# Optimization experiments

Measured on AMD Instinct MI355X. Metric: run time of the kernel, lower is better.

Reference implementation:

```python
import jax, jax.numpy as jnp
import numpy as np
from jax import lax

B, T, BYTE_LEN, EMB = 8, 4096, 8, 64
FILTERS = [(1, 4), (2, 8), (3, 12), (4, 16), (5, 20), (6, 24), (7, 28)]
LAST_DIM = sum(c for _, c in FILTERS)  # 112
OUT_DIM = 512


def setup_inputs() -> dict:
    key = jax.random.key(0)
    ks = jax.random.split(key, 32)
    inp = {"features": jax.random.normal(ks[0], (B, T, BYTE_LEN, EMB), dtype=jnp.float32)}
    for i, (w, c) in enumerate(FILTERS):
        inp[f"conv_w{i+1}"] = jax.random.normal(ks[1 + i], (c, EMB, w), dtype=jnp.float32) * 0.05
        inp[f"conv_b{i+1}"] = jax.random.normal(ks[8 + i], (c,), dtype=jnp.float32) * 0.05
    inp["hw_w1"] = jax.random.normal(ks[15], (2 * LAST_DIM, LAST_DIM), dtype=jnp.float32) * 0.05
    inp["hw_b1"] = jnp.concatenate([jnp.zeros(LAST_DIM), jnp.ones(LAST_DIM)]).astype(jnp.float32)
    inp["hw_w2"] = jax.random.normal(ks[16], (2 * LAST_DIM, LAST_DIM), dtype=jnp.float32) * 0.05
    inp["hw_b2"] = jnp.concatenate([jnp.zeros(LAST_DIM), jnp.ones(LAST_DIM)]).astype(jnp.float32)
    inp["proj_w"] = jax.random.normal(ks[17], (OUT_DIM, LAST_DIM), dtype=jnp.float32) * 0.05
    inp["proj_b"] = jax.random.normal(ks[18], (OUT_DIM,), dtype=jnp.float32) * 0.05
    return inp


def _conv_branch(x, w, b):
    # x: [N, EMB, BYTE_LEN], w: [out_c, EMB, width] -> max over time, relu -> [N, out_c]
    y = lax.conv_general_dilated(x, w, window_strides=(1,), padding='VALID',
                                 dimension_numbers=('NCH', 'OIH', 'NCH'))
    y = y + b[None, :, None]
    return jax.nn.relu(jnp.max(y, axis=-1))


def _highway_layer(x, w, b):
    p = x @ w.T + b
    proj_x, gate = jnp.split(p, 2, axis=-1)
    g = jax.nn.sigmoid(gate)
    return g * x + (1.0 - g) * jax.nn.relu(proj_x)


def reference(features, conv_w1, conv_w2, conv_w3, conv_w4, conv_w5, conv_w6, conv_w7,
              conv_b1, conv_b2, conv_b3, conv_b4, conv_b5, conv_b6, conv_b7,
              hw_w1, hw_b1, hw_w2, hw_b2, proj_w, proj_b):
    b, t, byte_len, emb = features.shape
    # transpose(2,3).view(-1, emb, byte_len)
    x = features.transpose(0, 1, 3, 2).reshape(-1, emb, byte_len)  # [B*T, EMB, BYTE_LEN]
    ws = [conv_w1, conv_w2, conv_w3, conv_w4, conv_w5, conv_w6, conv_w7]
    bs = [conv_b1, conv_b2, conv_b3, conv_b4, conv_b5, conv_b6, conv_b7]
    branches = [_conv_branch(x, w, bb) for w, bb in zip(ws, bs)]
    h = jnp.concatenate(branches, axis=-1)  # [B*T, LAST_DIM]
    h = _highway_layer(h, hw_w1, hw_b1)
    h = _highway_layer(h, hw_w2, hw_b2)
    out = h @ proj_w.T + proj_b  # [B*T, OUT_DIM]
    return out.reshape(b, t, -1)
```

## Files before the change

kernel.cpp:

```cpp
#include <hip/hip_runtime.h>

typedef __attribute__((ext_vector_type(8))) short short8;
typedef __attribute__((ext_vector_type(4))) float f32x4;

#define KDIM 512
#define NCT  30
#define CB_STRIDE 97
#define HT_OFF    28672
#define HT_STRIDE 132
#define RING_CH   8192

__device__ __forceinline__ unsigned short f2bf(float x) {
    unsigned u = __float_as_uint(x);
    return (unsigned short)((u + 0x7FFFu + ((u >> 16) & 1u)) >> 16);
}
__device__ __forceinline__ float bf2f(unsigned short h) {
    return __uint_as_float(((unsigned)h) << 16);
}

__device__ __forceinline__ void stage16(const void* g, void* l, int lane) {
    __builtin_amdgcn_global_load_lds(
        (const __attribute__((address_space(1))) unsigned int*)g,
        (__attribute__((address_space(3))) unsigned int*)l, 16, 0, 0);
}

__global__ void prep_kernel(const float* __restrict__ w1, const float* __restrict__ w2,
                            const float* __restrict__ w3, const float* __restrict__ w4,
                            const float* __restrict__ w5, const float* __restrict__ w6,
                            const float* __restrict__ w7, const float* __restrict__ hw1,
                            const float* __restrict__ hw2, const float* __restrict__ pw,
                            unsigned short* __restrict__ WC, unsigned short* __restrict__ W1s,
                            unsigned short* __restrict__ W2s, unsigned short* __restrict__ Ps) {
    int gid = blockIdx.x * 256 + threadIdx.x;
    if (gid < 245760) {
        int k = gid / 480, col = gid % 480;
        const float* wp; int cbnd, NP, C, W;
        if (col < 32)       { wp = w1; cbnd = 0;   NP = 8; C = 4;  W = 1; }
        else if (col < 96)  { wp = w2; cbnd = 32;  NP = 7; C = 8;  W = 2; }
        else if (col < 176) { wp = w3; cbnd = 96;  NP = 6; C = 12; W = 3; }
        else if (col < 256) { wp = w4; cbnd = 176; NP = 5; C = 16; W = 4; }
        else if (col < 336) { wp = w5; cbnd = 256; NP = 4; C = 20; W = 5; }
        else if (col < 416) { wp = w6; cbnd = 336; NP = 3; C = 24; W = 6; }
        else                { wp = w7; cbnd = 416; NP = 2; C = 28; W = 7; }
        int c2 = col - cbnd, oc = c2 / NP, p = c2 - oc * NP;
        int j = k >> 6, e = k & 63, dk = j - p;
        float v = 0.f;
        if (oc < C && dk >= 0 && dk < W) v = wp[(oc * 64 + e) * W + dk];
        int q = k >> 5, kr = k & 31;
        WC[q * 16384 + ((col >> 4) * 64 + ((kr >> 3) * 16 + (col & 15))) * 8 + (kr & 7)] = f2bf(v);
    } else if (gid < 245760 + 57344) {
        int x = gid - 245760;
        const float* src = (x < 28672) ? hw1 : hw2;
        unsigned short* dst = (x < 28672) ? W1s : W2s;
        if (x >= 28672) x -= 28672;
        int k = x / 224, n = x % 224;
        float v = (k < 112) ? src[n * 112 + k] : 0.f;
        int q = k >> 5, kr = k & 31;
        int h = (n >= 112) ? 1 : 0;
        int tt = (n >> 4) - h * 7;
        dst[(q * 2 + h) * 4096 + (tt * 64 + ((kr >> 3) * 16 + (n & 15))) * 8 + (kr & 7)] = f2bf(v);
    } else if (gid < 245760 + 57344 + 65536) {
        int x = gid - 303104;
        int k = x / 512, n = x % 512;
        float v = (k < 112) ? pw[n * 112 + k] : 0.f;
        int q = k >> 5, kr = k & 31;
        int c = q * 4 + (n >> 7);
        int tt = (n >> 4) & 7;
        Ps[c * 4096 + (tt * 64 + ((kr >> 3) * 16 + (n & 15))) * 8 + (kr & 7)] = f2bf(v);
    }
}

template <int T0, int NT>
__device__ __forceinline__ void dump_phase(float* Cb, const f32x4* acc, int w4, int lane) {
    int r0 = w4 * 16 + ((lane >> 4) * 4);
    int c0 = lane & 15;
#pragma unroll
    for (int tt = 0; tt < NT; ++tt)
#pragma unroll
        for (int r = 0; r < 4; ++r)
            Cb[(r0 + r) * CB_STRIDE + tt * 16 + c0] = acc[T0 + tt][r];
}

__device__ void reduce_phase(const float* Cb, unsigned short* ht, int tid,
                             int cA, int NPA, int choffA, int colbA, const float* cbA,
                             int cB, int NPB, int choffB, int colbB, const float* cbB) {
    int noc = cA + cB;
    for (int idx = tid; idx < 64 * noc; idx += 512) {
        int row = idx & 63, ocp = idx >> 6;
        bool isB = ocp >= cA;
        int oc = isB ? ocp - cA : ocp;
        int NP = isB ? NPB : NPA;
        int colb = isB ? colbB : colbA;
        int choff = isB ? choffB : choffA;
        const float* cb = isB ? cbB : cbA;
        const float* src = Cb + row * CB_STRIDE + colb + oc * NP;
        float m = src[0];
        for (int k = 1; k < NP; ++k) m = fmaxf(m, src[k]);
        float v = fmaxf(m + cb[oc], 0.f);
        ht[row * HT_STRIDE + choff + oc] = f2bf(v);
    }
}

template <int T0, int NT>
__device__ __forceinline__ void epi_phase(float* Cb, unsigned short* ht, const f32x4* acc,
                                          int tid, int wave, int lane,
                                          int cA, int NPA, int choffA, int colbA, const float* cbA,
                                          int cB, int NPB, int choffB, int colbB, const float* cbB) {
    for (int g = 0; g < 2; ++g) {
        if ((wave >> 2) == g) dump_phase<T0, NT>(Cb, acc, wave & 3, lane);
        __syncthreads();
        reduce_phase(Cb, ht + g * 64 * HT_STRIDE, tid,
                     cA, NPA, choffA, colbA, cbA, cB, NPB, choffB, colbB, cbB);
        __syncthreads();
    }
}

__global__ __launch_bounds__(512, 2) void fused_kernel(
        const float* __restrict__ feat, const unsigned short* __restrict__ WC,
        const float* cb0, const float* cb1, const float* cb2, const float* cb3,
        const float* cb4, const float* cb5, const float* cb6,
        const unsigned short* __restrict__ W1, const unsigned short* __restrict__ W2,
        const unsigned short* __restrict__ PW,
        const float* __restrict__ hb1, const float* __restrict__ hb2,
        const float* __restrict__ pb, float* __restrict__ out) {
    __shared__ __align__(16) char sm[65536];
    const int tid = threadIdx.x, lane = tid & 63, wave = tid >> 6;
    const int c0 = lane & 15, kq = lane >> 4;
    const int m0 = blockIdx.x * 128;
    f32x4 zero = {0.f, 0.f, 0.f, 0.f};

    const float* arow = feat + (size_t)(m0 + wave * 16 + c0) * KDIM + kq * 8;
    short8 af[16];
#pragma unroll
    for (int q = 0; q < 16; ++q) {
        float t[8];
        *(float4*)(t)     = *(const float4*)(arow + q * 32);
        *(float4*)(t + 4) = *(const float4*)(arow + q * 32 + 4);
        short8 v;
#pragma unroll
        for (int i = 0; i < 8; ++i) v[i] = (short)f2bf(t[i]);
        af[q] = v;
    }

    f32x4 acc[NCT];
#pragma unroll
    for (int t = 0; t < NCT; ++t) acc[t] = zero;

    for (int i = tid; i < 2048; i += 512)
        stage16(WC + i * 8, sm + (i - lane) * 16, lane);

#pragma unroll
    for (int q = 0; q < 16; ++q) {
        if (q < 15) {
            const unsigned short* src = WC + (q + 1) * 16384;
            char* dst = sm + ((q + 1) & 1) * 32768;
            for (int i = tid; i < 2048; i += 512)
                stage16(src + i * 8, dst + (i - lane) * 16, lane);
            asm volatile("s_waitcnt vmcnt(4)" ::: "memory");
        } else {
            asm volatile("s_waitcnt vmcnt(0)" ::: "memory");
        }
        __builtin_amdgcn_s_barrier();
        const char* bb = sm + (q & 1) * 32768;
#pragma unroll
        for (int t = 0; t < NCT; ++t) {
            short8 b = *(const short8*)(bb + (t * 64 + lane) * 16);
            acc[t] = __builtin_amdgcn_mfma_f32_16x16x32_bf16(af[q], b, acc[t], 0, 0, 0);
        }
        asm volatile("s_waitcnt lgkmcnt(0)" ::: "memory");
        __builtin_amdgcn_s_barrier();
    }

    float* Cb = (float*)sm;
    unsigned short* ht = (unsigned short*)(sm + HT_OFF);
    for (int i = tid; i < 2048; i += 512)
        ht[(i >> 4) * HT_STRIDE + 112 + (i & 15)] = 0;
    __syncthreads();
    epi_phase<0, 6>(Cb, ht, acc, tid, wave, lane, 4, 8, 0, 0, cb0, 8, 7, 4, 32, cb1);
    epi_phase<6, 5>(Cb, ht, acc, tid, wave, lane, 12, 6, 12, 0, cb2, 0, 1, 0, 0, cb2);
    epi_phase<11, 5>(Cb, ht, acc, tid, wave, lane, 16, 5, 24, 0, cb3, 0, 1, 0, 0, cb3);
    epi_phase<16, 5>(Cb, ht, acc, tid, wave, lane, 20, 4, 40, 0, cb4, 0, 1, 0, 0, cb4);
    epi_phase<21, 5>(Cb, ht, acc, tid, wave, lane, 24, 3, 60, 0, cb5, 0, 1, 0, 0, cb5);
    epi_phase<26, 4>(Cb, ht, acc, tid, wave, lane, 28, 2, 84, 0, cb6, 0, 1, 0, 0, cb6);

    char* ring = sm;
    short8 a2[4];
#pragma unroll
    for (int q = 0; q < 4; ++q)
        a2[q] = *(const short8*)((const char*)ht + (wave * 16 + c0) * 264 + q * 64 + kq * 16);

    stage16(W1 + tid * 8, ring + (tid - lane) * 16, lane);
    stage16(W1 + 4096 + tid * 8, ring + RING_CH + (tid - lane) * 16, lane);

    f32x4 acc2[14];
#pragma unroll
    for (int t = 0; t < 14; ++t) acc2[t] = zero;
#pragma unroll
    for (int i = 0; i < 8; ++i) {
        {
            const unsigned short* src = (i < 6) ? (W1 + (i + 2) * 4096) : (W2 + (i - 6) * 4096);
            char* dst = ring + ((i + 2) % 3) * RING_CH;
            stage16(src + tid * 8, dst + (tid - lane) * 16, lane);
        }
        asm volatile("s_waitcnt vmcnt(2)" ::: "memory");
        __builtin_amdgcn_s_barrier();
        const char* bb = ring + (i % 3) * RING_CH;
        const int q = i >> 1, h = i & 1;
#pragma unroll
        for (int tt = 0; tt < 7; ++tt) {
            short8 b = *(const short8*)(bb + (tt * 64 + lane) * 16);
            acc2[h * 7 + tt] = __builtin_amdgcn_mfma_f32_16x16x32_bf16(a2[q], b, acc2[h * 7 + tt], 0, 0, 0);
        }
        asm volatile("s_waitcnt lgkmcnt(0)" ::: "memory");
        __builtin_amdgcn_s_barrier();
    }

#pragma unroll
    for (int t = 0; t < 14; ++t) {
        float bp = hb1[t * 16 + c0], bg = hb1[112 + t * 16 + c0];
        (void)bg;
#pragma unroll
        for (int r = 0; r < 4; ++r) {
            int row = wave * 16 + kq * 4 + r;
            int col = t * 16 + c0;
            if (t < 7) {
                float px = acc2[t][r] + bp;
                float gt = acc2[t + 7][r] + hb1[112 + t * 16 + c0];
                float g = 1.f / (1.f + __expf(-gt));
                float hres = bf2f(ht[row * HT_STRIDE + col]);
                ht[row * HT_STRIDE + col] = f2bf(g * hres + (1.f - g) * fmaxf(px, 0.f));
            }
        }
    }
    asm volatile("s_waitcnt lgkmcnt(0)" ::: "memory");
    __builtin_amdgcn_s_barrier();

    short8 a3[4];
#pragma unroll
    for (int q = 0; q < 4; ++q)
        a3[q] = *(const short8*)((const char*)ht + (wave * 16 + c0) * 264 + q * 64 + kq * 16);

    f32x4 acc3[14];
#pragma unroll
    for (int t = 0; t < 14; ++t) acc3[t] = zero;
#pragma unroll
    for (int j = 0; j < 8; ++j) {
        {
            const unsigned short* src = (j < 6) ? (W2 + (j + 2) * 4096) : (PW + (j - 6) * 4096);
            char* dst = ring + ((j + 10) % 3) * RING_CH;
            stage16(src + tid * 8, dst + (tid - lane) * 16, lane);
        }
        asm volatile("s_waitcnt vmcnt(2)" ::: "memory");
        __builtin_amdgcn_s_barrier();
        const char* bb = ring + ((j + 8) % 3) * RING_CH;
        const int q = j >> 1, h = j & 1;
#pragma unroll
        for (int tt = 0; tt < 7; ++tt) {
            short8 b = *(const short8*)(bb + (tt * 64 + lane) * 16);
            acc3[h * 7 + tt] = __builtin_amdgcn_mfma_f32_16x16x32_bf16(a3[q], b, acc3[h * 7 + tt], 0, 0, 0);
        }
        asm volatile("s_waitcnt lgkmcnt(0)" ::: "memory");
        __builtin_amdgcn_s_barrier();
    }

#pragma unroll
    for (int t = 0; t < 7; ++t) {
        float bp = hb2[t * 16 + c0], bg = hb2[112 + t * 16 + c0];
#pragma unroll
        for (int r = 0; r < 4; ++r) {
            int row = wave * 16 + kq * 4 + r;
            int col = t * 16 + c0;
            float px = acc3[t][r] + bp;
            float gt = acc3[t + 7][r] + bg;
            float g = 1.f / (1.f + __expf(-gt));
            float hres = bf2f(ht[row * HT_STRIDE + col]);
            ht[row * HT_STRIDE + col] = f2bf(g * hres + (1.f - g) * fmaxf(px, 0.f));
        }
    }
    asm volatile("s_waitcnt lgkmcnt(0)" ::: "memory");
    __builtin_amdgcn_s_barrier();

    short8 a4[4];
#pragma unroll
    for (int q = 0; q < 4; ++q)
        a4[q] = *(const short8*)((const char*)ht + (wave * 16 + c0) * 264 + q * 64 + kq * 16);

    f32x4 acc4[32];
#pragma unroll
    for (int t = 0; t < 32; ++t) acc4[t] = zero;
#pragma unroll
    for (int k = 0; k < 16; ++k) {
        if (k < 14) {
            const unsigned short* src = PW + (k + 2) * 4096;
            char* dst = ring + ((k + 18) % 3) * RING_CH;
            stage16(src + tid * 8, dst + (tid - lane) * 16, lane);
            asm volatile("s_waitcnt vmcnt(2)" ::: "memory");
        } else if (k == 14) {
            asm volatile("s_waitcnt vmcnt(1)" ::: "memory");
        } else {
            asm volatile("s_waitcnt vmcnt(0)" ::: "memory");
        }
        __builtin_amdgcn_s_barrier();
        const char* bb = ring + ((k + 16) % 3) * RING_CH;
        const int q = k >> 2, e = k & 3;
#pragma unroll
        for (int tt = 0; tt < 8; ++tt) {
            short8 b = *(const short8*)(bb + (tt * 64 + lane) * 16);
            acc4[e * 8 + tt] = __builtin_amdgcn_mfma_f32_16x16x32_bf16(a4[q], b, acc4[e * 8 + tt], 0, 0, 0);
        }
        asm volatile("s_waitcnt lgkmcnt(0)" ::: "memory");
        __builtin_amdgcn_s_barrier();
    }

    float* ot = (float*)sm;
#pragma unroll
    for (int e = 0; e < 4; ++e) {
        __syncthreads();
#pragma unroll
        for (int tt = 0; tt < 8; ++tt) {
            int col = e * 128 + tt * 16 + c0;
            float b = pb[col];
#pragma unroll
            for (int r = 0; r < 4; ++r)
                ot[(wave * 16 + kq * 4 + r) * 128 + tt * 16 + c0] = acc4[e * 8 + tt][r] + b;
        }
        __syncthreads();
        for (int i = tid; i < 4096; i += 512) {
            int row = i >> 5, c = i & 31;
            *(float4*)(out + (size_t)(m0 + row) * 512 + e * 128 + c * 4) = ((const float4*)ot)[i];
        }
    }
}

extern "C" void kernel_launch(void* const* d_in, const int* in_sizes, int n_in,
                              void* d_out, int out_size, void* d_ws, size_t ws_size,
                              hipStream_t stream) {
    const float* feat = (const float*)d_in[0];
    const float* cw[7];
    const float* cb[7];
    for (int f = 0; f < 7; ++f) {
        cw[f] = (const float*)d_in[1 + 2 * f];
        cb[f] = (const float*)d_in[2 + 2 * f];
    }
    const float* hw_w1 = (const float*)d_in[15];
    const float* hw_b1 = (const float*)d_in[16];
    const float* hw_w2 = (const float*)d_in[17];
    const float* hw_b2 = (const float*)d_in[18];
    const float* pw    = (const float*)d_in[19];
    const float* pb    = (const float*)d_in[20];
    float* out = (float*)d_out;

    char* ws = (char*)d_ws;
    unsigned short* WC  = (unsigned short*)ws;
    unsigned short* W1s = (unsigned short*)(ws + 524288);
    unsigned short* W2s = (unsigned short*)(ws + 589824);
    unsigned short* Ps  = (unsigned short*)(ws + 655360);

    prep_kernel<<<1440, 256, 0, stream>>>(cw[0], cw[1], cw[2], cw[3], cw[4], cw[5], cw[6],
                                          hw_w1, hw_w2, pw, WC, W1s, W2s, Ps);
    fused_kernel<<<256, 512, 0, stream>>>(feat, WC, cb[0], cb[1], cb[2], cb[3], cb[4], cb[5], cb[6],
                                          W1s, W2s, Ps, hw_b1, hw_b2, pb, out);
}
```

Baseline: 191.7 us.

## Deepen conv weight pipeline, stage whole highway/proj weights in large LDS

The conv GEMM now keeps a 4-slot LDS ring with two chunks in flight instead of double-buffering, which drops the trailing barrier each iteration. The highway and projection weights are repacked into contiguous tiles and loaded whole into a 145KB dynamic LDS allocation, overlapping their loads with the conv epilogue and earlier layers. The aim is to remove most per-chunk barriers and load stalls. The output is now written straight from registers instead of being restaged through LDS. The large LDS footprint limits each CU to one block, down from two, and the direct output stores are less coalesced.

After: 198.7 us. 3.7% more time.

```diff
diff --git a/kernel.cpp b/kernel.cpp
--- a/kernel.cpp
+++ b/kernel.cpp
@@ -5,10 +5,14 @@
 
 #define KDIM 512
 #define NCT  30
-#define CB_STRIDE 97
-#define HT_OFF    28672
+#define SLOT      32768
+#define W1_OFF    0
+#define W2_OFF    57344
+#define CB_OFF    93952
+#define HT_OFF    114688
+#define LDS_TOTAL 148480
 #define HT_STRIDE 132
-#define RING_CH   8192
+#define CBS 81
 
 __device__ __forceinline__ unsigned short f2bf(float x) {
     unsigned u = __float_as_uint(x);
@@ -56,17 +60,13 @@
         int k = x / 224, n = x % 224;
         float v = (k < 112) ? src[n * 112 + k] : 0.f;
         int q = k >> 5, kr = k & 31;
-        int h = (n >= 112) ? 1 : 0;
-        int tt = (n >> 4) - h * 7;
-        dst[(q * 2 + h) * 4096 + (tt * 64 + ((kr >> 3) * 16 + (n & 15))) * 8 + (kr & 7)] = f2bf(v);
+        dst[(q * 14 + (n >> 4)) * 512 + ((kr >> 3) * 16 + (n & 15)) * 8 + (kr & 7)] = f2bf(v);
     } else if (gid < 245760 + 57344 + 65536) {
         int x = gid - 303104;
         int k = x / 512, n = x % 512;
         float v = (k < 112) ? pw[n * 112 + k] : 0.f;
         int q = k >> 5, kr = k & 31;
-        int c = q * 4 + (n >> 7);
-        int tt = (n >> 4) & 7;
-        Ps[c * 4096 + (tt * 64 + ((kr >> 3) * 16 + (n & 15))) * 8 + (kr & 7)] = f2bf(v);
+        Ps[(q * 32 + (n >> 4)) * 512 + ((kr >> 3) * 16 + (n & 15)) * 8 + (kr & 7)] = f2bf(v);
     }
 }
 
@@ -78,40 +78,33 @@
     for (int tt = 0; tt < NT; ++tt)
 #pragma unroll
         for (int r = 0; r < 4; ++r)
-            Cb[(r0 + r) * CB_STRIDE + tt * 16 + c0] = acc[T0 + tt][r];
-}
-
-__device__ void reduce_phase(const float* Cb, unsigned short* ht, int tid,
-                             int cA, int NPA, int choffA, int colbA, const float* cbA,
-                             int cB, int NPB, int choffB, int colbB, const float* cbB) {
-    int noc = cA + cB;
-    for (int idx = tid; idx < 64 * noc; idx += 512) {
-        int row = idx & 63, ocp = idx >> 6;
-        bool isB = ocp >= cA;
-        int oc = isB ? ocp - cA : ocp;
-        int NP = isB ? NPB : NPA;
-        int colb = isB ? colbB : colbA;
-        int choff = isB ? choffB : choffA;
-        const float* cb = isB ? cbB : cbA;
-        const float* src = Cb + row * CB_STRIDE + colb + oc * NP;
+            Cb[(r0 + r) * CBS + tt * 16 + c0] = acc[T0 + tt][r];
+}
+
+__device__ __forceinline__ void reduce_rows(const float* Cb, unsigned short* ht, int tid,
+                                            int c, int NP, int choff, const float* cb) {
+    for (int idx = tid; idx < 64 * c; idx += 512) {
+        int row = idx & 63, oc = idx >> 6;
+        const float* src = Cb + row * CBS + oc * NP;
         float m = src[0];
         for (int k = 1; k < NP; ++k) m = fmaxf(m, src[k]);
-        float v = fmaxf(m + cb[oc], 0.f);
-        ht[row * HT_STRIDE + choff + oc] = f2bf(v);
+        ht[row * HT_STRIDE + choff + oc] = f2bf(fmaxf(m + cb[oc], 0.f));
     }
 }
 
 template <int T0, int NT>
-__device__ __forceinline__ void epi_phase(float* Cb, unsigned short* ht, const f32x4* acc,
-                                          int tid, int wave, int lane,
-                                          int cA, int NPA, int choffA, int colbA, const float* cbA,
-                                          int cB, int NPB, int choffB, int colbB, const float* cbB) {
+__device__ __forceinline__ void epi_phase(char* smb, const f32x4* acc, int tid, int wave, int lane,
+                                          int c, int NP, int choff, const float* cb) {
+    float* Cb = (float*)(smb + CB_OFF);
+    unsigned short* ht = (unsigned short*)(smb + HT_OFF);
+#pragma unroll
     for (int g = 0; g < 2; ++g) {
         if ((wave >> 2) == g) dump_phase<T0, NT>(Cb, acc, wave & 3, lane);
-        __syncthreads();
-        reduce_phase(Cb, ht + g * 64 * HT_STRIDE, tid,
-                     cA, NPA, choffA, colbA, cbA, cB, NPB, choffB, colbB, cbB);
-        __syncthreads();
+        asm volatile("s_waitcnt lgkmcnt(0)" ::: "memory");
+        __builtin_amdgcn_s_barrier();
+        reduce_rows(Cb, ht + g * 64 * HT_STRIDE, tid, c, NP, choff, cb);
+        asm volatile("s_waitcnt lgkmcnt(0)" ::: "memory");
+        __builtin_amdgcn_s_barrier();
     }
 }
 
@@ -123,11 +116,12 @@
         const unsigned short* __restrict__ PW,
         const float* __restrict__ hb1, const float* __restrict__ hb2,
         const float* __restrict__ pb, float* __restrict__ out) {
-    __shared__ __align__(16) char sm[65536];
+    extern __shared__ __align__(16) char sm[];
     const int tid = threadIdx.x, lane = tid & 63, wave = tid >> 6;
     const int c0 = lane & 15, kq = lane >> 4;
     const int m0 = blockIdx.x * 128;
     f32x4 zero = {0.f, 0.f, 0.f, 0.f};
+    unsigned short* ht = (unsigned short*)(sm + HT_OFF);
 
     const float* arow = feat + (size_t)(m0 + wave * 16 + c0) * KDIM + kq * 8;
     short8 af[16];
@@ -148,120 +142,104 @@
 
     for (int i = tid; i < 2048; i += 512)
         stage16(WC + i * 8, sm + (i - lane) * 16, lane);
+    for (int i = tid; i < 2048; i += 512)
+        stage16(WC + 16384 + i * 8, sm + SLOT + (i - lane) * 16, lane);
 
 #pragma unroll
     for (int q = 0; q < 16; ++q) {
-        if (q < 15) {
-            const unsigned short* src = WC + (q + 1) * 16384;
-            char* dst = sm + ((q + 1) & 1) * 32768;
+        if (q < 14) {
+            const unsigned short* src = WC + (q + 2) * 16384;
+            char* dst = sm + ((q + 2) & 3) * SLOT;
             for (int i = tid; i < 2048; i += 512)
                 stage16(src + i * 8, dst + (i - lane) * 16, lane);
+            asm volatile("s_waitcnt vmcnt(8)" ::: "memory");
+        } else if (q == 14) {
             asm volatile("s_waitcnt vmcnt(4)" ::: "memory");
         } else {
             asm volatile("s_waitcnt vmcnt(0)" ::: "memory");
         }
         __builtin_amdgcn_s_barrier();
-        const char* bb = sm + (q & 1) * 32768;
+        const char* bb = sm + (q & 3) * SLOT;
 #pragma unroll
         for (int t = 0; t < NCT; ++t) {
             short8 b = *(const short8*)(bb + (t * 64 + lane) * 16);
             acc[t] = __builtin_amdgcn_mfma_f32_16x16x32_bf16(af[q], b, acc[t], 0, 0, 0);
         }
-        asm volatile("s_waitcnt lgkmcnt(0)" ::: "memory");
-        __builtin_amdgcn_s_barrier();
-    }
-
-    float* Cb = (float*)sm;
-    unsigned short* ht = (unsigned short*)(sm + HT_OFF);
+    }
+    asm volatile("s_waitcnt lgkmcnt(0)" ::: "memory");
+    __builtin_amdgcn_s_barrier();
+
+    for (int i = tid; i < 3584; i += 512)
+        stage16(W1 + i * 8, sm + W1_OFF + (i - lane) * 16, lane);
+
     for (int i = tid; i < 2048; i += 512)
         ht[(i >> 4) * HT_STRIDE + 112 + (i & 15)] = 0;
-    __syncthreads();
-    epi_phase<0, 6>(Cb, ht, acc, tid, wave, lane, 4, 8, 0, 0, cb0, 8, 7, 4, 32, cb1);
-    epi_phase<6, 5>(Cb, ht, acc, tid, wave, lane, 12, 6, 12, 0, cb2, 0, 1, 0, 0, cb2);
-    epi_phase<11, 5>(Cb, ht, acc, tid, wave, lane, 16, 5, 24, 0, cb3, 0, 1, 0, 0, cb3);
-    epi_phase<16, 5>(Cb, ht, acc, tid, wave, lane, 20, 4, 40, 0, cb4, 0, 1, 0, 0, cb4);
-    epi_phase<21, 5>(Cb, ht, acc, tid, wave, lane, 24, 3, 60, 0, cb5, 0, 1, 0, 0, cb5);
-    epi_phase<26, 4>(Cb, ht, acc, tid, wave, lane, 28, 2, 84, 0, cb6, 0, 1, 0, 0, cb6);
-
-    char* ring = sm;
+
+    epi_phase<0, 2>(sm, acc, tid, wave, lane, 4, 8, 0, cb0);
+    epi_phase<2, 4>(sm, acc, tid, wave, lane, 8, 7, 4, cb1);
+    epi_phase<6, 5>(sm, acc, tid, wave, lane, 12, 6, 12, cb2);
+    epi_phase<11, 5>(sm, acc, tid, wave, lane, 16, 5, 24, cb3);
+    epi_phase<16, 5>(sm, acc, tid, wave, lane, 20, 4, 40, cb4);
+    epi_phase<21, 5>(sm, acc, tid, wave, lane, 24, 3, 60, cb5);
+    epi_phase<26, 4>(sm, acc, tid, wave, lane, 28, 2, 84, cb6);
+
     short8 a2[4];
 #pragma unroll
     for (int q = 0; q < 4; ++q)
-        a2[q] = *(const short8*)((const char*)ht + (wave * 16 + c0) * 264 + q * 64 + kq * 16);
-
-    stage16(W1 + tid * 8, ring + (tid - lane) * 16, lane);
-    stage16(W1 + 4096 + tid * 8, ring + RING_CH + (tid - lane) * 16, lane);
+        a2[q] = *(const short8*)((const char*)ht + (wave * 16 + c0) * (HT_STRIDE * 2) + q * 64 + kq * 16);
+
+    for (int i = tid; i < 3584; i += 512)
+        stage16(W2 + i * 8, sm + W2_OFF + (i - lane) * 16, lane);
+    asm volatile("s_waitcnt vmcnt(7)" ::: "memory");
+    __builtin_amdgcn_s_barrier();
 
     f32x4 acc2[14];
 #pragma unroll
     for (int t = 0; t < 14; ++t) acc2[t] = zero;
 #pragma unroll
-    for (int i = 0; i < 8; ++i) {
-        {
-            const unsigned short* src = (i < 6) ? (W1 + (i + 2) * 4096) : (W2 + (i - 6) * 4096);
-            char* dst = ring + ((i + 2) % 3) * RING_CH;
-            stage16(src + tid * 8, dst + (tid - lane) * 16, lane);
-        }
-        asm volatile("s_waitcnt vmcnt(2)" ::: "memory");
-        __builtin_amdgcn_s_barrier();
-        const char* bb = ring + (i % 3) * RING_CH;
-        const int q = i >> 1, h = i & 1;
-#pragma unroll
-        for (int tt = 0; tt < 7; ++tt) {
-            short8 b = *(const short8*)(bb + (tt * 64 + lane) * 16);
-            acc2[h * 7 + tt] = __builtin_amdgcn_mfma_f32_16x16x32_bf16(a2[q], b, acc2[h * 7 + tt], 0, 0, 0);
-        }
-        asm volatile("s_waitcnt lgkmcnt(0)" ::: "memory");
-        __builtin_amdgcn_s_barrier();
-    }
-
-#pragma unroll
-    for (int t = 0; t < 14; ++t) {
+    for (int q = 0; q < 4; ++q)
+#pragma unroll
+        for (int t = 0; t < 14; ++t) {
+            short8 b = *(const short8*)(sm + W1_OFF + (q * 14 + t) * 1024 + lane * 16);
+            acc2[t] = __builtin_amdgcn_mfma_f32_16x16x32_bf16(a2[q], b, acc2[t], 0, 0, 0);
+        }
+
+#pragma unroll
+    for (int t = 0; t < 7; ++t) {
         float bp = hb1[t * 16 + c0], bg = hb1[112 + t * 16 + c0];
-        (void)bg;
 #pragma unroll
         for (int r = 0; r < 4; ++r) {
             int row = wave * 16 + kq * 4 + r;
             int col = t * 16 + c0;
-            if (t < 7) {
-                float px = acc2[t][r] + bp;
-                float gt = acc2[t + 7][r] + hb1[112 + t * 16 + c0];
-                float g = 1.f / (1.f + __expf(-gt));
-                float hres = bf2f(ht[row * HT_STRIDE + col]);
-                ht[row * HT_STRIDE + col] = f2bf(g * hres + (1.f - g) * fmaxf(px, 0.f));
-            }
-        }
-    }
-    asm volatile("s_waitcnt lgkmcnt(0)" ::: "memory");
+            float px = acc2[t][r] + bp;
+            float gt = acc2[t + 7][r] + bg;
+            float g = 1.f / (1.f + __expf(-gt));
+            float hres = bf2f(ht[row * HT_STRIDE + col]);
+            ht[row * HT_STRIDE + col] = f2bf(g * hres + (1.f - g) * fmaxf(px, 0.f));
+        }
+    }
+
+    short8 a3[4];
+#pragma unroll
+    for (int q = 0; q < 4; ++q)
+        a3[q] = *(const short8*)((const char*)ht + (wave * 16 + c0) * (HT_STRIDE * 2) + q * 64 + kq * 16);
+
+    asm volatile("s_waitcnt vmcnt(0)" ::: "memory");
     __builtin_amdgcn_s_barrier();
 
-    short8 a3[4];
-#pragma unroll
-    for (int q = 0; q < 4; ++q)
-        a3[q] = *(const short8*)((const char*)ht + (wave * 16 + c0) * 264 + q * 64 + kq * 16);
+    for (int i = tid; i < 2048; i += 512)
+        stage16(PW + i * 8, sm + (i - lane) * 16, lane);
 
     f32x4 acc3[14];
 #pragma unroll
     for (int t = 0; t < 14; ++t) acc3[t] = zero;
 #pragma unroll
-    for (int j = 0; j < 8; ++j) {
-        {
-            const unsigned short* src = (j < 6) ? (W2 + (j + 2) * 4096) : (PW + (j - 6) * 4096);
-            char* dst = ring + ((j + 10) % 3) * RING_CH;
-            stage16(src + tid * 8, dst + (tid - lane) * 16, lane);
-        }
-        asm volatile("s_waitcnt vmcnt(2)" ::: "memory");
-        __builtin_amdgcn_s_barrier();
-        const char* bb = ring + ((j + 8) % 3) * RING_CH;
-        const int q = j >> 1, h = j & 1;
-#pragma unroll
-        for (int tt = 0; tt < 7; ++tt) {
-            short8 b = *(const short8*)(bb + (tt * 64 + lane) * 16);
-            acc3[h * 7 + tt] = __builtin_amdgcn_mfma_f32_16x16x32_bf16(a3[q], b, acc3[h * 7 + tt], 0, 0, 0);
-        }
-        asm volatile("s_waitcnt lgkmcnt(0)" ::: "memory");
-        __builtin_amdgcn_s_barrier();
-    }
+    for (int q = 0; q < 4; ++q)
+#pragma unroll
+        for (int t = 0; t < 14; ++t) {
+            short8 b = *(const short8*)(sm + W2_OFF + (q * 14 + t) * 1024 + lane * 16);
+            acc3[t] = __builtin_amdgcn_mfma_f32_16x16x32_bf16(a3[q], b, acc3[t], 0, 0, 0);
+        }
 
 #pragma unroll
     for (int t = 0; t < 7; ++t) {
@@ -277,58 +255,45 @@
             ht[row * HT_STRIDE + col] = f2bf(g * hres + (1.f - g) * fmaxf(px, 0.f));
         }
     }
+
+    short8 a4[4];
+#pragma unroll
+    for (int q = 0; q < 4; ++q)
+        a4[q] = *(const short8*)((const char*)ht + (wave * 16 + c0) * (HT_STRIDE * 2) + q * 64 + kq * 16);
+
     asm volatile("s_waitcnt lgkmcnt(0)" ::: "memory");
     __builtin_amdgcn_s_barrier();
 
-    short8 a4[4];
-#pragma unroll
-    for (int q = 0; q < 4; ++q)
-        a4[q] = *(const short8*)((const char*)ht + (wave * 16 + c0) * 264 + q * 64 + kq * 16);
+#pragma unroll
+    for (int c = 1; c < 4; ++c)
+        for (int i = tid; i < 2048; i += 512)
+            stage16(PW + c * 16384 + i * 8, sm + c * SLOT + (i - lane) * 16, lane);
 
     f32x4 acc4[32];
 #pragma unroll
     for (int t = 0; t < 32; ++t) acc4[t] = zero;
 #pragma unroll
-    for (int k = 0; k < 16; ++k) {
-        if (k < 14) {
-            const unsigned short* src = PW + (k + 2) * 4096;
-            char* dst = ring + ((k + 18) % 3) * RING_CH;
-            stage16(src + tid * 8, dst + (tid - lane) * 16, lane);
-            asm volatile("s_waitcnt vmcnt(2)" ::: "memory");
-        } else if (k == 14) {
-            asm volatile("s_waitcnt vmcnt(1)" ::: "memory");
-        } else {
-            asm volatile("s_waitcnt vmcnt(0)" ::: "memory");
-        }
+    for (int c = 0; c < 4; ++c) {
+        if (c == 0)      asm volatile("s_waitcnt vmcnt(12)" ::: "memory");
+        else if (c == 1) asm volatile("s_waitcnt vmcnt(8)" ::: "memory");
+        else if (c == 2) asm volatile("s_waitcnt vmcnt(4)" ::: "memory");
+        else             asm volatile("s_waitcnt vmcnt(0)" ::: "memory");
         __builtin_amdgcn_s_barrier();
-        const char* bb = ring + ((k + 16) % 3) * RING_CH;
-        const int q = k >> 2, e = k & 3;
-#pragma unroll
-        for (int tt = 0; tt < 8; ++tt) {
-            short8 b = *(const short8*)(bb + (tt * 64 + lane) * 16);
-            acc4[e * 8 + tt] = __builtin_amdgcn_mfma_f32_16x16x32_bf16(a4[q], b, acc4[e * 8 + tt], 0, 0, 0);
-        }
-        asm volatile("s_waitcnt lgkmcnt(0)" ::: "memory");
-        __builtin_amdgcn_s_barrier();
-    }
-
-    float* ot = (float*)sm;
-#pragma unroll
-    for (int e = 0; e < 4; ++e) {
-        __syncthreads();
-#pragma unroll
-        for (int tt = 0; tt < 8; ++tt) {
-            int col = e * 128 + tt * 16 + c0;
-            float b = pb[col];
-#pragma unroll
-            for (int r = 0; r < 4; ++r)
-                ot[(wave * 16 + kq * 4 + r) * 128 + tt * 16 + c0] = acc4[e * 8 + tt][r] + b;
-        }
-        __syncthreads();
-        for (int i = tid; i < 4096; i += 512) {
-            int row = i >> 5, c = i & 31;
-            *(float4*)(out + (size_t)(m0 + row) * 512 + e * 128 + c * 4) = ((const float4*)ot)[i];
-        }
+        const char* bb = sm + c * SLOT;
+#pragma unroll
+        for (int tt = 0; tt < 32; ++tt) {
+            short8 b = *(const short8*)(bb + tt * 1024 + lane * 16);
+            acc4[tt] = __builtin_amdgcn_mfma_f32_16x16x32_bf16(a4[c], b, acc4[tt], 0, 0, 0);
+        }
+    }
+
+    const int rbase = m0 + wave * 16 + kq * 4;
+#pragma unroll
+    for (int tt = 0; tt < 32; ++tt) {
+        float b = pb[tt * 16 + c0];
+#pragma unroll
+        for (int r = 0; r < 4; ++r)
+            out[(size_t)(rbase + r) * 512 + tt * 16 + c0] = acc4[tt][r] + b;
     }
 }
 
@@ -353,11 +318,14 @@
     char* ws = (char*)d_ws;
     unsigned short* WC  = (unsigned short*)ws;
     unsigned short* W1s = (unsigned short*)(ws + 524288);
-    unsigned short* W2s = (unsigned short*)(ws + 589824);
-    unsigned short* Ps  = (unsigned short*)(ws + 655360);
+    unsigned short* W2s = (unsigned short*)(ws + 581632);
+    unsigned short* Ps  = (unsigned short*)(ws + 638976);
+
+    hipFuncSetAttribute((const void*)fused_kernel,
+                        hipFuncAttributeMaxDynamicSharedMemorySize, LDS_TOTAL);
 
     prep_kernel<<<1440, 256, 0, stream>>>(cw[0], cw[1], cw[2], cw[3], cw[4], cw[5], cw[6],
                                           hw_w1, hw_w2, pw, WC, W1s, W2s, Ps);
-    fused_kernel<<<256, 512, 0, stream>>>(feat, WC, cb[0], cb[1], cb[2], cb[3], cb[4], cb[5], cb[6],
-                                          W1s, W2s, Ps, hw_b1, hw_b2, pb, out);
-}
+    fused_kernel<<<256, 512, LDS_TOTAL, stream>>>(feat, WC, cb[0], cb[1], cb[2], cb[3], cb[4],
+                                                  cb[5], cb[6], W1s, W2s, Ps, hw_b1, hw_b2, pb, out);
+}
```
